# Kernel tuning notes

Measured on AMD Instinct MI355X. Metric: run time of the kernel, lower is better.

## Reference

```python
import jax, jax.numpy as jnp
import numpy as np

NEG_SLOPE = 0.2
EPS = 1e-16


def gat_conv(x, edge_index, W, att_src, att_dst, bias, heads, out_ch, concat):
    """PyG-style GATConv (eval mode, add_self_loops=True)."""
    N = x.shape[0]
    h = (x @ W).reshape(N, heads, out_ch)              # [N,H,C]
    loop = jnp.arange(N, dtype=edge_index.dtype)
    src = jnp.concatenate([edge_index[0], loop])       # [E+N]
    dst = jnp.concatenate([edge_index[1], loop])
    a_src = jnp.sum(h * att_src, axis=-1)              # [N,H]
    a_dst = jnp.sum(h * att_dst, axis=-1)
    e = jax.nn.leaky_relu(a_src[src] + a_dst[dst], NEG_SLOPE)  # [E+N,H]
    # segment softmax over destination nodes
    m = jax.ops.segment_max(e, dst, num_segments=N)
    e = jnp.exp(e - m[dst])
    s = jax.ops.segment_sum(e, dst, num_segments=N)
    alpha = e / (s[dst] + EPS)                         # [E+N,H]
    msg = h[src] * alpha[..., None]                    # [E+N,H,C]
    out = jax.ops.segment_sum(msg, dst, num_segments=N)  # [N,H,C]
    out = out.reshape(N, heads * out_ch) if concat else out.mean(axis=1)
    return out + bias


def setup_inputs() -> dict:
    key = jax.random.key(0)
    ks = jax.random.split(key, 11)
    N, F, E = 100000, 128, 1600000
    H1, C1 = 4, 16
    H2, C2 = 1, 16
    return {
        "x": jax.random.normal(ks[0], (N, F), dtype=jnp.float32),
        "edge_index": jax.random.randint(ks[1], (2, E), 0, N, dtype=jnp.int64) if jax.config.jax_enable_x64 else jax.random.randint(ks[1], (2, E), 0, N).astype(jnp.int32),
        "W1": jax.random.normal(ks[2], (F, H1 * C1), dtype=jnp.float32) * 0.1,
        "att_src1": jax.random.normal(ks[3], (H1, C1), dtype=jnp.float32) * 0.1,
        "att_dst1": jax.random.normal(ks[4], (H1, C1), dtype=jnp.float32) * 0.1,
        "bias1": jax.random.normal(ks[5], (H1 * C1,), dtype=jnp.float32) * 0.1,
        "W2": jax.random.normal(ks[6], (H1 * C1, H2 * C2), dtype=jnp.float32) * 0.1,
        "att_src2": jax.random.normal(ks[7], (H2, C2), dtype=jnp.float32) * 0.1,
        "att_dst2": jax.random.normal(ks[8], (H2, C2), dtype=jnp.float32) * 0.1,
        "bias2": jax.random.normal(ks[9], (C2,), dtype=jnp.float32) * 0.1,
    }


def reference(x, edge_index, W1, att_src1, att_dst1, bias1, W2, att_src2, att_dst2, bias2):
    # dropout is identity in eval mode
    h = gat_conv(x, edge_index, W1, att_src1, att_dst1, bias1, heads=4, out_ch=16, concat=True)
    h = jax.nn.elu(h)
    h = gat_conv(h, edge_index, W2, att_src2, att_dst2, bias2, heads=1, out_ch=16, concat=False)
    return jax.nn.log_softmax(h, axis=1)
```

## Files before the change

kernel.cpp:

```cpp
#include <hip/hip_runtime.h>
#include <hip/hip_fp16.h>
#include <hip/hip_bf16.h>
#include <math.h>


#define BSH 8
#define BCAP 5120
#define CHK 4096

typedef __attribute__((ext_vector_type(8))) short short8;
typedef __attribute__((ext_vector_type(8))) _Float16 half8;
typedef __attribute__((ext_vector_type(4))) _Float16 half4;
typedef __attribute__((ext_vector_type(4))) float float4v;

static __device__ __forceinline__ short f2bf(float f) {
    __hip_bfloat16 b = __float2bfloat16(f);
    return *reinterpret_cast<short*>(&b);
}

__global__ __launch_bounds__(256) void k_init(int* __restrict__ cursor, int NBK,
                                              const float* __restrict__ W1,
                                              const float* __restrict__ att_src1,
                                              const float* __restrict__ att_dst1,
                                              short* __restrict__ wtg) {
    int tid = threadIdx.x;
    if (blockIdx.x == 0) {
        for (int i = tid; i < NBK; i += 256) cursor[i] = 0;
    } else {
        for (int i = tid; i < 128 * 64; i += 256) {
            int k = i >> 6, c = i & 63;
            wtg[c * 136 + k] = f2bf(W1[i]);
        }
        for (int i = tid; i < 16 * 128; i += 256) {
            int col = i >> 7, k = i & 127;
            float v = 0.f;
            if (col < 8) {
                int h = col & 3;
                const float* att = (col < 4) ? att_src1 : att_dst1;
                #pragma unroll
                for (int c = 0; c < 16; c++) v += W1[k * 64 + h * 16 + c] * att[h * 16 + c];
            }
            wtg[(64 + col) * 136 + k] = f2bf(v);
        }
    }
}

__global__ __launch_bounds__(256) void k_pre(const int* __restrict__ ei, int* __restrict__ cursor,
                                             int* __restrict__ stage, int E, int NBK,
                                             const float* __restrict__ x,
                                             const short* __restrict__ wtg,
                                             __half* __restrict__ h1,
                                             float* __restrict__ a_src, float* __restrict__ a_dst,
                                             int N, int GS) {
    __shared__ __align__(16) char smem[80 * 136 * 2];
    int tid = threadIdx.x;
    if (blockIdx.x < GS) {
        int* hist = (int*)smem;
        int* cnt2 = hist + 512;
        int* base = cnt2 + 512;
        int e0 = blockIdx.x * CHK;
        int nedge = E - e0; if (nedge > CHK) nedge = CHK;
        int nv4 = nedge >> 2, rem = nedge & 3;
        const int4* dv4 = (const int4*)(ei + E + e0);
        const int4* sv4 = (const int4*)(ei + e0);
        for (int i = tid; i < 512; i += 256) { hist[i] = 0; cnt2[i] = 0; }
        __syncthreads();
        for (int i = tid; i < nv4; i += 256) {
            int4 d = dv4[i];
            atomicAdd(&hist[d.x >> BSH], 1);
            atomicAdd(&hist[d.y >> BSH], 1);
            atomicAdd(&hist[d.z >> BSH], 1);
            atomicAdd(&hist[d.w >> BSH], 1);
        }
        if (tid < rem) atomicAdd(&hist[ei[E + e0 + nv4 * 4 + tid] >> BSH], 1);
        __syncthreads();
        for (int b = tid; b < NBK; b += 256) {
            int c = hist[b];
            if (c > 0) base[b] = b * BCAP + atomicAdd(&cursor[b], c);
        }
        __syncthreads();
        for (int i = tid; i < nv4; i += 256) {
            int4 s = sv4[i];
            int4 d = dv4[i];
            int b, r;
            b = d.x >> BSH; r = atomicAdd(&cnt2[b], 1);
            stage[base[b] + r] = s.x | ((d.x & 255) << 17);
            b = d.y >> BSH; r = atomicAdd(&cnt2[b], 1);
            stage[base[b] + r] = s.y | ((d.y & 255) << 17);
            b = d.z >> BSH; r = atomicAdd(&cnt2[b], 1);
            stage[base[b] + r] = s.z | ((d.z & 255) << 17);
            b = d.w >> BSH; r = atomicAdd(&cnt2[b], 1);
            stage[base[b] + r] = s.w | ((d.w & 255) << 17);
        }
        if (tid < rem) {
            int e = nv4 * 4 + tid;
            int s = ei[e0 + e];
            int d = ei[E + e0 + e];
            int b = d >> BSH;
            int r = atomicAdd(&cnt2[b], 1);
            stage[base[b] + r] = s | ((d & 255) << 17);
        }
    } else {
        short* wt = (short*)smem;
        {
            int4* wd = (int4*)wt;
            const int4* ws = (const int4*)wtg;
            for (int i = tid; i < (80 * 136 * 2) / 16; i += 256) wd[i] = ws[i];
        }
        __syncthreads();
        int wave = tid >> 6, lane = tid & 63;
        int m = lane & 15, q = lane >> 4;
        int nbase = (blockIdx.x - GS) * 64 + wave * 16;
        int anode = nbase + m;
        bool rowok = anode < N;
        const float* xrow = x + (size_t)(rowok ? anode : 0) * 128 + q * 8;

        float4v acc[5];
        #pragma unroll
        for (int ct = 0; ct < 5; ct++)
            #pragma unroll
            for (int r = 0; r < 4; r++) acc[ct][r] = 0.f;

        #pragma unroll
        for (int kc = 0; kc < 4; kc++) {
            float4 u0 = make_float4(0.f, 0.f, 0.f, 0.f), u1 = u0;
            if (rowok) {
                u0 = *(const float4*)(xrow + kc * 32);
                u1 = *(const float4*)(xrow + kc * 32 + 4);
            }
            short8 af;
            af[0] = f2bf(u0.x); af[1] = f2bf(u0.y); af[2] = f2bf(u0.z); af[3] = f2bf(u0.w);
            af[4] = f2bf(u1.x); af[5] = f2bf(u1.y); af[6] = f2bf(u1.z); af[7] = f2bf(u1.w);
            #pragma unroll
            for (int ct = 0; ct < 5; ct++) {
                short8 bf = *(const short8*)&wt[(ct * 16 + m) * 136 + kc * 32 + q * 8];
                acc[ct] = __builtin_amdgcn_mfma_f32_16x16x32_bf16(af, bf, acc[ct], 0, 0, 0);
            }
        }
        #pragma unroll
        for (int ct = 0; ct < 4; ct++) {
            #pragma unroll
            for (int r = 0; r < 4; r++) {
                int n = nbase + q * 4 + r;
                if (n < N) h1[(size_t)n * 64 + ct * 16 + m] = __float2half(acc[ct][r]);
            }
        }
        #pragma unroll
        for (int r = 0; r < 4; r++) {
            int n = nbase + q * 4 + r;
            if (n < N) {
                float v = acc[4][r];
                if (m < 4) a_src[n * 4 + m] = v;
                else if (m < 8) a_dst[n * 4 + (m - 4)] = v;
            }
        }
    }
}

__global__ __launch_bounds__(256) void k_build(const int* __restrict__ stage,
                                               const int* __restrict__ cursor,
                                               int* __restrict__ row_start,
                                               int* __restrict__ csr,
                                               int NBK, int E, int N) {
    __shared__ int cnt[256];
    __shared__ int lb[256];
    __shared__ int cur[256];
    __shared__ int sA[256];
    int b = blockIdx.x, tid = threadIdx.x;
    int nodes0 = b << BSH;
    int nnodes = N - nodes0; if (nnodes > 256) nnodes = 256;
    int partial = 0;
    for (int i = tid; i < b; i += 256) partial += cursor[i];
    sA[tid] = partial;
    __syncthreads();
    for (int off = 128; off >= 1; off >>= 1) {
        if (tid < off) sA[tid] += sA[tid + off];
        __syncthreads();
    }
    int ebase = sA[0];
    int ecnt = cursor[b];
    __syncthreads();
    if (b == 0 && tid == 0) row_start[N] = E + N;
    const int* sbk = stage + b * BCAP;
    cnt[tid] = (tid < nnodes) ? 1 : 0;
    __syncthreads();
    int e4 = ecnt & ~3;
    for (int e = tid * 4; e < e4; e += 1024) {
        int4 v = *(const int4*)&sbk[e];
        atomicAdd(&cnt[(v.x >> 17) & 255], 1);
        atomicAdd(&cnt[(v.y >> 17) & 255], 1);
        atomicAdd(&cnt[(v.z >> 17) & 255], 1);
        atomicAdd(&cnt[(v.w >> 17) & 255], 1);
    }
    if (tid < (ecnt & 3)) atomicAdd(&cnt[(sbk[e4 + tid] >> 17) & 255], 1);
    __syncthreads();
    int myc = cnt[tid];
    sA[tid] = myc;
    __syncthreads();
    for (int off = 1; off < 256; off <<= 1) {
        int r = sA[tid] + ((tid >= off) ? sA[tid - off] : 0);
        __syncthreads();
        sA[tid] = r;
        __syncthreads();
    }
    int gb = ebase + nodes0;
    lb[tid] = sA[tid] - myc;
    cur[tid] = 1;
    __syncthreads();
    if (tid < nnodes) {
        row_start[nodes0 + tid] = gb + lb[tid];
        csr[gb + lb[tid]] = nodes0 + tid;
    }
    __syncthreads();
    for (int e = tid * 4; e < e4; e += 1024) {
        int4 v = *(const int4*)&sbk[e];
        int l, r;
        l = (v.x >> 17) & 255; r = atomicAdd(&cur[l], 1); csr[gb + lb[l] + r] = v.x & 0x1FFFF;
        l = (v.y >> 17) & 255; r = atomicAdd(&cur[l], 1); csr[gb + lb[l] + r] = v.y & 0x1FFFF;
        l = (v.z >> 17) & 255; r = atomicAdd(&cur[l], 1); csr[gb + lb[l] + r] = v.z & 0x1FFFF;
        l = (v.w >> 17) & 255; r = atomicAdd(&cur[l], 1); csr[gb + lb[l] + r] = v.w & 0x1FFFF;
    }
    if (tid < (ecnt & 3)) {
        int v = sbk[e4 + tid];
        int l = (v >> 17) & 255;
        int r = atomicAdd(&cur[l], 1);
        csr[gb + lb[l] + r] = v & 0x1FFFF;
    }
}

__global__ __launch_bounds__(256) void k_agg1f(const int* __restrict__ row_start,
                                               const int* __restrict__ csr_src,
                                               const float* __restrict__ a_src,
                                               const float* __restrict__ a_dst,
                                               const __half* __restrict__ h1,
                                               const float* __restrict__ bias,
                                               const float* __restrict__ W2,
                                               const float* __restrict__ att_src2,
                                               const float* __restrict__ att_dst2,
                                               __half* __restrict__ h2,
                                               float* __restrict__ a_src2,
                                               float* __restrict__ a_dst2, int N) {
    __shared__ float sW2[64 * 17];
    __shared__ float sAs[16], sAd[16];
    int tid = threadIdx.x;
    for (int i = tid; i < 1024; i += 256) sW2[(i >> 4) * 17 + (i & 15)] = W2[i];
    if (tid < 16) { sAs[tid] = att_src2[tid]; sAd[tid] = att_dst2[tid]; }
    __syncthreads();
    int wave = tid >> 6, lane = tid & 63;
    int grp = lane >> 3, sub = lane & 3, par = (lane >> 2) & 1;
    int node = blockIdx.x * 32 + wave * 8 + grp;
    if (node >= N) return;
    int row = row_start[node];
    int deg = row_start[node + 1] - row;
    float adm = a_dst[node * 4 + sub];
    const _Float16* hb = (const _Float16*)h1 + sub * 16;
    const int* cp = csr_src + row + par;
    float A[16];
    #pragma unroll
    for (int c = 0; c < 16; c++) A[c] = 0.f;
    float sh = 0.f;
    int c0 = 0, c1 = 0, c2 = 0, c3 = 0;
    if (deg >= 8) { c0 = cp[0]; c1 = cp[2]; c2 = cp[4]; c3 = cp[6]; }
    int j = 0;
    for (; j + 8 <= deg; j += 8) {
        int s0 = c0, s1 = c1, s2 = c2, s3 = c3;
        float x0 = a_src[s0 * 4 + sub] + adm;
        float x1 = a_src[s1 * 4 + sub] + adm;
        float x2 = a_src[s2 * 4 + sub] + adm;
        float x3 = a_src[s3 * 4 + sub] + adm;
        half8 p0 = *(const half8*)(hb + (size_t)s0 * 64);
        half8 q0 = *(const half8*)(hb + (size_t)s0 * 64 + 8);
        half8 p1 = *(const half8*)(hb + (size_t)s1 * 64);
        half8 q1 = *(const half8*)(hb + (size_t)s1 * 64 + 8);
        half8 p2 = *(const half8*)(hb + (size_t)s2 * 64);
        half8 q2 = *(const half8*)(hb + (size_t)s2 * 64 + 8);
        half8 p3 = *(const half8*)(hb + (size_t)s3 * 64);
        half8 q3 = *(const half8*)(hb + (size_t)s3 * 64 + 8);
        if (j + 16 <= deg) {
            c0 = cp[j + 8]; c1 = cp[j + 10]; c2 = cp[j + 12]; c3 = cp[j + 14];
        }
        float e0 = __expf(fmaxf(x0, 0.2f * x0));
        float e1 = __expf(fmaxf(x1, 0.2f * x1));
        float e2 = __expf(fmaxf(x2, 0.2f * x2));
        float e3 = __expf(fmaxf(x3, 0.2f * x3));
        sh += (e0 + e1) + (e2 + e3);
        #pragma unroll
        for (int c = 0; c < 8; c++) {
            A[c]     += e0 * (float)p0[c] + e1 * (float)p1[c]
                      + e2 * (float)p2[c] + e3 * (float)p3[c];
            A[c + 8] += e0 * (float)q0[c] + e1 * (float)q1[c]
                      + e2 * (float)q2[c] + e3 * (float)q3[c];
        }
    }
    for (; j < deg; j += 2) {
        int idx = j + par;
        if (idx < deg) {
            int s = csr_src[row + idx];
            float xv = a_src[s * 4 + sub] + adm;
            half8 p = *(const half8*)(hb + (size_t)s * 64);
            half8 q = *(const half8*)(hb + (size_t)s * 64 + 8);
            float e = __expf(fmaxf(xv, 0.2f * xv));
            sh += e;
            #pragma unroll
            for (int c = 0; c < 8; c++) {
                A[c]     += e * (float)p[c];
                A[c + 8] += e * (float)q[c];
            }
        }
    }
    sh += __shfl_xor(sh, 4, 64);
    #pragma unroll
    for (int c = 0; c < 16; c++) A[c] += __shfl_xor(A[c], 4, 64);
    float iv = 1.f / (sh + 1e-16f);
    const float4* bb = (const float4*)bias + sub * 4;
    float o[16];
    #pragma unroll
    for (int c4 = 0; c4 < 4; c4++) {
        float4 b = bb[c4];
        float o0 = A[c4 * 4 + 0] * iv + b.x;
        float o1 = A[c4 * 4 + 1] * iv + b.y;
        float o2 = A[c4 * 4 + 2] * iv + b.z;
        float o3 = A[c4 * 4 + 3] * iv + b.w;
        o[c4 * 4 + 0] = (o0 > 0.f) ? o0 : (__expf(o0) - 1.f);
        o[c4 * 4 + 1] = (o1 > 0.f) ? o1 : (__expf(o1) - 1.f);
        o[c4 * 4 + 2] = (o2 > 0.f) ? o2 : (__expf(o2) - 1.f);
        o[c4 * 4 + 3] = (o3 > 0.f) ? o3 : (__expf(o3) - 1.f);
    }
    float pk[8];
    #pragma unroll
    for (int kk = 0; kk < 8; kk++) pk[kk] = 0.f;
    #pragma unroll
    for (int cc = 0; cc < 16; cc++) {
        float ov = o[cc];
        const float* wr = &sW2[(sub * 16 + cc) * 17 + par * 8];
        #pragma unroll
        for (int kk = 0; kk < 8; kk++) pk[kk] += ov * wr[kk];
    }
    #pragma unroll
    for (int kk = 0; kk < 8; kk++) {
        pk[kk] += __shfl_xor(pk[kk], 1, 64);
        pk[kk] += __shfl_xor(pk[kk], 2, 64);
    }
    if (sub == 0) {
        union { __half2 hh[4]; float4 f; } u;
        u.hh[0] = __floats2half2_rn(pk[0], pk[1]);
        u.hh[1] = __floats2half2_rn(pk[2], pk[3]);
        u.hh[2] = __floats2half2_rn(pk[4], pk[5]);
        u.hh[3] = __floats2half2_rn(pk[6], pk[7]);
        *(float4*)&h2[(size_t)node * 16 + par * 8] = u.f;
    }
    float ps = 0.f, pd = 0.f;
    #pragma unroll
    for (int kk = 0; kk < 8; kk++) {
        ps += pk[kk] * sAs[par * 8 + kk];
        pd += pk[kk] * sAd[par * 8 + kk];
    }
    ps += __shfl_xor(ps, 4, 64);
    pd += __shfl_xor(pd, 4, 64);
    if (sub == 0 && par == 0) { a_src2[node] = ps; a_dst2[node] = pd; }
}

__global__ __launch_bounds__(256) void k_agg2(const int* __restrict__ row_start,
                                              const int* __restrict__ csr_src,
                                              const float* __restrict__ a_src,
                                              const float* __restrict__ a_dst,
                                              const __half* __restrict__ h2,
                                              const float* __restrict__ bias,
                                              float* __restrict__ out, int N) {
    int tid = threadIdx.x;
    int wave = tid >> 6, lane = tid & 63;
    int grp = lane >> 3, sub = lane & 3, par = (lane >> 2) & 1;
    int node = blockIdx.x * 32 + wave * 8 + grp;
    if (node >= N) return;
    int row = row_start[node];
    int deg = row_start[node + 1] - row;
    float ad = a_dst[node];
    const _Float16* hb = (const _Float16*)h2 + sub * 4;
    const int* cp = csr_src + row + par;
    float A0 = 0.f, A1 = 0.f, A2 = 0.f, A3 = 0.f;
    float sh = 0.f;
    int c0 = 0, c1 = 0, c2 = 0, c3 = 0;
    if (deg >= 8) { c0 = cp[0]; c1 = cp[2]; c2 = cp[4]; c3 = cp[6]; }
    int j = 0;
    for (; j + 8 <= deg; j += 8) {
        int s0 = c0, s1 = c1, s2 = c2, s3 = c3;
        float x0 = a_src[s0] + ad;
        float x1 = a_src[s1] + ad;
        float x2 = a_src[s2] + ad;
        float x3 = a_src[s3] + ad;
        half4 v0 = *(const half4*)(hb + (size_t)s0 * 16);
        half4 v1 = *(const half4*)(hb + (size_t)s1 * 16);
        half4 v2 = *(const half4*)(hb + (size_t)s2 * 16);
        half4 v3 = *(const half4*)(hb + (size_t)s3 * 16);
        if (j + 16 <= deg) {
            c0 = cp[j + 8]; c1 = cp[j + 10]; c2 = cp[j + 12]; c3 = cp[j + 14];
        }
        float e0 = __expf(fmaxf(x0, 0.2f * x0));
        float e1 = __expf(fmaxf(x1, 0.2f * x1));
        float e2 = __expf(fmaxf(x2, 0.2f * x2));
        float e3 = __expf(fmaxf(x3, 0.2f * x3));
        sh += (e0 + e1) + (e2 + e3);
        A0 += e0 * (float)v0[0] + e1 * (float)v1[0] + e2 * (float)v2[0] + e3 * (float)v3[0];
        A1 += e0 * (float)v0[1] + e1 * (float)v1[1] + e2 * (float)v2[1] + e3 * (float)v3[1];
        A2 += e0 * (float)v0[2] + e1 * (float)v1[2] + e2 * (float)v2[2] + e3 * (float)v3[2];
        A3 += e0 * (float)v0[3] + e1 * (float)v1[3] + e2 * (float)v2[3] + e3 * (float)v3[3];
    }
    for (; j < deg; j += 2) {
        int idx = j + par;
        if (idx < deg) {
            int s = csr_src[row + idx];
            float xv = a_src[s] + ad;
            half4 v = *(const half4*)(hb + (size_t)s * 16);
            float e = __expf(fmaxf(xv, 0.2f * xv));
            sh += e;
            A0 += e * (float)v[0];
            A1 += e * (float)v[1];
            A2 += e * (float)v[2];
            A3 += e * (float)v[3];
        }
    }
    sh += __shfl_xor(sh, 4, 64);
    A0 += __shfl_xor(A0, 4, 64);
    A1 += __shfl_xor(A1, 4, 64);
    A2 += __shfl_xor(A2, 4, 64);
    A3 += __shfl_xor(A3, 4, 64);
    float iv = 1.f / (sh + 1e-16f);
    float4 b = ((const float4*)bias)[sub];
    float v0 = A0 * iv + b.x;
    float v1 = A1 * iv + b.y;
    float v2 = A2 * iv + b.z;
    float v3 = A3 * iv + b.w;
    float mx = fmaxf(fmaxf(v0, v1), fmaxf(v2, v3));
    mx = fmaxf(mx, __shfl_xor(mx, 1, 64));
    mx = fmaxf(mx, __shfl_xor(mx, 2, 64));
    float se = __expf(v0 - mx) + __expf(v1 - mx) + __expf(v2 - mx) + __expf(v3 - mx);
    se += __shfl_xor(se, 1, 64);
    se += __shfl_xor(se, 2, 64);
    float ls = mx + __logf(se);
    if (par == 0)
        *(float4*)&out[(size_t)node * 16 + sub * 4] =
            make_float4(v0 - ls, v1 - ls, v2 - ls, v3 - ls);
}

extern "C" void kernel_launch(void* const* d_in, const int* in_sizes, int n_in,
                              void* d_out, int out_size, void* d_ws, size_t ws_size,
                              hipStream_t stream) {
    const float* x        = (const float*)d_in[0];
    const int*   ei       = (const int*)d_in[1];
    const float* W1       = (const float*)d_in[2];
    const float* att_src1 = (const float*)d_in[3];
    const float* att_dst1 = (const float*)d_in[4];
    const float* bias1    = (const float*)d_in[5];
    const float* W2       = (const float*)d_in[6];
    const float* att_src2 = (const float*)d_in[7];
    const float* att_dst2 = (const float*)d_in[8];
    const float* bias2    = (const float*)d_in[9];
    float* out = (float*)d_out;

    const int N = in_sizes[0] / 128;
    const int E = in_sizes[1] / 2;
    const int NBK = (N + 255) >> BSH;
    const int GS = (E + CHK - 1) / CHK;
    const int GG = (N + 63) / 64;

    char* p = (char*)d_ws;
    auto alloc = [&](size_t bytes) -> void* {
        void* r = (void*)p;
        p += (bytes + 255) & ~(size_t)255;
        return r;
    };
    __half* h1     = (__half*)alloc((size_t)N * 64 * 2);
    __half* h2     = (__half*)alloc((size_t)N * 16 * 2);
    float* a_src1  = (float*)alloc((size_t)N * 4 * 4);
    float* a_dst1  = (float*)alloc((size_t)N * 4 * 4);
    float* a_src2  = (float*)alloc((size_t)N * 4);
    float* a_dst2  = (float*)alloc((size_t)N * 4);
    int*   row_st  = (int*)alloc((size_t)(N + 1) * 4);
    int*   csr     = (int*)alloc((size_t)(E + N) * 4);
    int*   stage   = (int*)alloc((size_t)NBK * BCAP * 4);
    int*   cursor  = (int*)alloc((size_t)NBK * 4);
    short* wtg     = (short*)alloc(80 * 136 * 2);
    (void)ws_size; (void)n_in; (void)out_size;

    k_init<<<2, 256, 0, stream>>>(cursor, NBK, W1, att_src1, att_dst1, wtg);
    k_pre<<<GS + GG, 256, 0, stream>>>(ei, cursor, stage, E, NBK,
                                       x, wtg, h1, a_src1, a_dst1, N, GS);
    k_build<<<NBK, 256, 0, stream>>>(stage, cursor, row_st, csr, NBK, E, N);
    k_agg1f<<<(N + 31) / 32, 256, 0, stream>>>(row_st, csr, a_src1, a_dst1, h1, bias1,
                                               W2, att_src2, att_dst2,
                                               h2, a_src2, a_dst2, N);
    k_agg2<<<(N + 31) / 32, 256, 0, stream>>>(row_st, csr, a_src2, a_dst2, h2, bias2, out, N);
}
```

Measured before the change: 230.0 us.

## Fold weight prep into GEMM blocks and split CSR build per half-bucket

Removes the separate init kernel: the cursor is cleared with an async memset and each GEMM block of k_pre builds its own bf16 transposed W1 and attention projection in shared memory. The CSR build kernel now launches two blocks per bucket, each owning 128 destination nodes, to raise parallelism. This trades a kernel launch and a global round-trip for redundant per-block weight preparation, and each build block still scans the whole bucket.

Measured after the change: 232.4 us. About the same (+1.0%).

```diff
diff --git a/kernel.cpp b/kernel.cpp
--- a/kernel.cpp
+++ b/kernel.cpp
@@ -18,37 +18,12 @@
     return *reinterpret_cast<short*>(&b);
 }
 
-__global__ __launch_bounds__(256) void k_init(int* __restrict__ cursor, int NBK,
-                                              const float* __restrict__ W1,
-                                              const float* __restrict__ att_src1,
-                                              const float* __restrict__ att_dst1,
-                                              short* __restrict__ wtg) {
-    int tid = threadIdx.x;
-    if (blockIdx.x == 0) {
-        for (int i = tid; i < NBK; i += 256) cursor[i] = 0;
-    } else {
-        for (int i = tid; i < 128 * 64; i += 256) {
-            int k = i >> 6, c = i & 63;
-            wtg[c * 136 + k] = f2bf(W1[i]);
-        }
-        for (int i = tid; i < 16 * 128; i += 256) {
-            int col = i >> 7, k = i & 127;
-            float v = 0.f;
-            if (col < 8) {
-                int h = col & 3;
-                const float* att = (col < 4) ? att_src1 : att_dst1;
-                #pragma unroll
-                for (int c = 0; c < 16; c++) v += W1[k * 64 + h * 16 + c] * att[h * 16 + c];
-            }
-            wtg[(64 + col) * 136 + k] = f2bf(v);
-        }
-    }
-}
-
 __global__ __launch_bounds__(256) void k_pre(const int* __restrict__ ei, int* __restrict__ cursor,
                                              int* __restrict__ stage, int E, int NBK,
                                              const float* __restrict__ x,
-                                             const short* __restrict__ wtg,
+                                             const float* __restrict__ W1,
+                                             const float* __restrict__ att_src1,
+                                             const float* __restrict__ att_dst1,
                                              __half* __restrict__ h1,
                                              float* __restrict__ a_src, float* __restrict__ a_dst,
                                              int N, int GS) {
@@ -102,10 +77,20 @@
         }
     } else {
         short* wt = (short*)smem;
-        {
-            int4* wd = (int4*)wt;
-            const int4* ws = (const int4*)wtg;
-            for (int i = tid; i < (80 * 136 * 2) / 16; i += 256) wd[i] = ws[i];
+        for (int i = tid; i < 128 * 64; i += 256) {
+            int k = i >> 6, c = i & 63;
+            wt[c * 136 + k] = f2bf(W1[i]);
+        }
+        for (int i = tid; i < 16 * 128; i += 256) {
+            int col = i >> 7, k = i & 127;
+            float v = 0.f;
+            if (col < 8) {
+                int h = col & 3;
+                const float* att = (col < 4) ? att_src1 : att_dst1;
+                #pragma unroll
+                for (int c = 0; c < 16; c++) v += W1[k * 64 + h * 16 + c] * att[h * 16 + c];
+            }
+            wt[(64 + col) * 136 + k] = f2bf(v);
         }
         __syncthreads();
         int wave = tid >> 6, lane = tid & 63;
@@ -157,18 +142,21 @@
     }
 }
 
-__global__ __launch_bounds__(256) void k_build(const int* __restrict__ stage,
-                                               const int* __restrict__ cursor,
-                                               int* __restrict__ row_start,
-                                               int* __restrict__ csr,
-                                               int NBK, int E, int N) {
-    __shared__ int cnt[256];
-    __shared__ int lb[256];
-    __shared__ int cur[256];
+__global__ __launch_bounds__(256) void k_build2(const int* __restrict__ stage,
+                                                const int* __restrict__ cursor,
+                                                int* __restrict__ row_start,
+                                                int* __restrict__ csr,
+                                                int NBK, int E, int N) {
+    __shared__ int cnt[128];
+    __shared__ int lb[128];
+    __shared__ int cur[128];
     __shared__ int sA[256];
-    int b = blockIdx.x, tid = threadIdx.x;
-    int nodes0 = b << BSH;
-    int nnodes = N - nodes0; if (nnodes > 256) nnodes = 256;
+    int blk = blockIdx.x, tid = threadIdx.x;
+    int b = blk >> 1, half = blk & 1;
+    int nodes0 = (b << BSH) + (half << 7);
+    int nnodes = N - nodes0;
+    if (nnodes > 128) nnodes = 128;
+    if (nnodes < 0) nnodes = 0;
     int partial = 0;
     for (int i = tid; i < b; i += 256) partial += cursor[i];
     sA[tid] = partial;
@@ -180,32 +168,42 @@
     int ebase = sA[0];
     int ecnt = cursor[b];
     __syncthreads();
-    if (b == 0 && tid == 0) row_start[N] = E + N;
+    if (b == 0 && half == 0 && tid == 0) row_start[N] = E + N;
     const int* sbk = stage + b * BCAP;
-    cnt[tid] = (tid < nnodes) ? 1 : 0;
-    __syncthreads();
+    if (tid < 128) cnt[tid] = (tid < nnodes) ? 1 : 0;
+    __syncthreads();
+    int hb = half << 7;
     int e4 = ecnt & ~3;
     for (int e = tid * 4; e < e4; e += 1024) {
         int4 v = *(const int4*)&sbk[e];
-        atomicAdd(&cnt[(v.x >> 17) & 255], 1);
-        atomicAdd(&cnt[(v.y >> 17) & 255], 1);
-        atomicAdd(&cnt[(v.z >> 17) & 255], 1);
-        atomicAdd(&cnt[(v.w >> 17) & 255], 1);
-    }
-    if (tid < (ecnt & 3)) atomicAdd(&cnt[(sbk[e4 + tid] >> 17) & 255], 1);
-    __syncthreads();
-    int myc = cnt[tid];
+        int l;
+        l = (v.x >> 17) & 255; if ((l & 128) == hb) atomicAdd(&cnt[l & 127], 1);
+        l = (v.y >> 17) & 255; if ((l & 128) == hb) atomicAdd(&cnt[l & 127], 1);
+        l = (v.z >> 17) & 255; if ((l & 128) == hb) atomicAdd(&cnt[l & 127], 1);
+        l = (v.w >> 17) & 255; if ((l & 128) == hb) atomicAdd(&cnt[l & 127], 1);
+    }
+    if (tid < (ecnt & 3)) {
+        int l = (sbk[e4 + tid] >> 17) & 255;
+        if ((l & 128) == hb) atomicAdd(&cnt[l & 127], 1);
+    }
+    __syncthreads();
+    int myc = (tid < 128) ? cnt[tid] : 0;
     sA[tid] = myc;
     __syncthreads();
-    for (int off = 1; off < 256; off <<= 1) {
+    for (int off = 1; off < 128; off <<= 1) {
         int r = sA[tid] + ((tid >= off) ? sA[tid - off] : 0);
         __syncthreads();
         sA[tid] = r;
         __syncthreads();
     }
-    int gb = ebase + nodes0;
-    lb[tid] = sA[tid] - myc;
-    cur[tid] = 1;
+    int own_width = sA[127];
+    int own_edges = own_width - nnodes;
+    int half0_edges = half ? (ecnt - own_edges) : 0;
+    int gb = ebase + half0_edges + nodes0;
+    if (tid < 128) {
+        lb[tid] = sA[tid] - myc;
+        cur[tid] = 1;
+    }
     __syncthreads();
     if (tid < nnodes) {
         row_start[nodes0 + tid] = gb + lb[tid];
@@ -215,16 +213,22 @@
     for (int e = tid * 4; e < e4; e += 1024) {
         int4 v = *(const int4*)&sbk[e];
         int l, r;
-        l = (v.x >> 17) & 255; r = atomicAdd(&cur[l], 1); csr[gb + lb[l] + r] = v.x & 0x1FFFF;
-        l = (v.y >> 17) & 255; r = atomicAdd(&cur[l], 1); csr[gb + lb[l] + r] = v.y & 0x1FFFF;
-        l = (v.z >> 17) & 255; r = atomicAdd(&cur[l], 1); csr[gb + lb[l] + r] = v.z & 0x1FFFF;
-        l = (v.w >> 17) & 255; r = atomicAdd(&cur[l], 1); csr[gb + lb[l] + r] = v.w & 0x1FFFF;
+        l = (v.x >> 17) & 255;
+        if ((l & 128) == hb) { r = atomicAdd(&cur[l & 127], 1); csr[gb + lb[l & 127] + r] = v.x & 0x1FFFF; }
+        l = (v.y >> 17) & 255;
+        if ((l & 128) == hb) { r = atomicAdd(&cur[l & 127], 1); csr[gb + lb[l & 127] + r] = v.y & 0x1FFFF; }
+        l = (v.z >> 17) & 255;
+        if ((l & 128) == hb) { r = atomicAdd(&cur[l & 127], 1); csr[gb + lb[l & 127] + r] = v.z & 0x1FFFF; }
+        l = (v.w >> 17) & 255;
+        if ((l & 128) == hb) { r = atomicAdd(&cur[l & 127], 1); csr[gb + lb[l & 127] + r] = v.w & 0x1FFFF; }
     }
     if (tid < (ecnt & 3)) {
         int v = sbk[e4 + tid];
         int l = (v >> 17) & 255;
-        int r = atomicAdd(&cur[l], 1);
-        csr[gb + lb[l] + r] = v & 0x1FFFF;
+        if ((l & 128) == hb) {
+            int r = atomicAdd(&cur[l & 127], 1);
+            csr[gb + lb[l & 127] + r] = v & 0x1FFFF;
+        }
     }
 }
 
@@ -479,13 +483,13 @@
     int*   csr     = (int*)alloc((size_t)(E + N) * 4);
     int*   stage   = (int*)alloc((size_t)NBK * BCAP * 4);
     int*   cursor  = (int*)alloc((size_t)NBK * 4);
-    short* wtg     = (short*)alloc(80 * 136 * 2);
     (void)ws_size; (void)n_in; (void)out_size;
 
-    k_init<<<2, 256, 0, stream>>>(cursor, NBK, W1, att_src1, att_dst1, wtg);
+    hipMemsetAsync(cursor, 0, (size_t)NBK * 4, stream);
     k_pre<<<GS + GG, 256, 0, stream>>>(ei, cursor, stage, E, NBK,
-                                       x, wtg, h1, a_src1, a_dst1, N, GS);
-    k_build<<<NBK, 256, 0, stream>>>(stage, cursor, row_st, csr, NBK, E, N);
+                                       x, W1, att_src1, att_dst1,
+                                       h1, a_src1, a_dst1, N, GS);
+    k_build2<<<NBK * 2, 256, 0, stream>>>(stage, cursor, row_st, csr, NBK, E, N);
     k_agg1f<<<(N + 31) / 32, 256, 0, stream>>>(row_st, csr, a_src1, a_dst1, h1, bias1,
                                                W2, att_src2, att_dst2,
                                                h2, a_src2, a_dst2, N);
```
